# Optimization experiments

Hardware: AMD Instinct MI355X
Metric: run time of the kernel (lower is better)

Reference implementation:

```python
import jax, jax.numpy as jnp
import numpy as np

B, T, D, H = 2, 2048, 1024, 16
DH = D // H
THETA = 10000.0
MAX_SEQ_LEN = 2048


def setup_inputs() -> dict:
    key = jax.random.key(0)
    kx, kqkv, ko = jax.random.split(key, 3)
    # trunc_normal init matching the torch Linear (std=sqrt(2/(fan_in+fan_out)), clipped at 3 sigma)
    sigma_qkv = (2.0 / (D + 3 * D)) ** 0.5
    sigma_o = (2.0 / (D + D)) ** 0.5
    W_qkv = jax.random.truncated_normal(kqkv, -3.0, 3.0, (3 * D, D), jnp.float32) * sigma_qkv
    W_o = jax.random.truncated_normal(ko, -3.0, 3.0, (D, D), jnp.float32) * sigma_o
    # RoPE caches: angles[t, i] = t / theta^(2i/d_k)
    dims = jnp.arange(0, DH, 2, dtype=jnp.float32)
    inv_freq = 1.0 / (THETA ** (dims / DH))  # [DH/2]
    angles = jnp.arange(MAX_SEQ_LEN, dtype=jnp.float32)[:, None] * inv_freq[None, :]  # [T, DH/2]
    return {
        "x": jax.random.normal(kx, (B, T, D), jnp.float32),
        "token_positions": jnp.arange(T, dtype=jnp.int64 if jax.config.jax_enable_x64 else jnp.int32),
        "W_qkv": W_qkv,
        "W_o": W_o,
        "cos_cached": jnp.cos(angles),
        "sin_cached": jnp.sin(angles),
    }


def _apply_rope(x, cos, sin):
    # x: [b, h, t, dh]; cos/sin: [t, dh/2] broadcast over (b, h)
    x1 = x[..., 0::2]
    x2 = x[..., 1::2]
    r1 = x1 * cos - x2 * sin
    r2 = x1 * sin + x2 * cos
    # interleave back: (.., dh/2, 2) -> (.., dh)
    return jnp.stack([r1, r2], axis=-1).reshape(x.shape)


def reference(x, token_positions, W_qkv, W_o, cos_cached, sin_cached):
    b, t, d = x.shape
    qkv = jnp.einsum("btd,ed->bte", x, W_qkv)  # [b, t, 3d]
    q, k, v = jnp.split(qkv, 3, axis=-1)

    def to_heads(z):
        return z.reshape(b, t, H, DH).transpose(0, 2, 1, 3)  # [b, h, t, dh]

    q, k, v = to_heads(q), to_heads(k), to_heads(v)

    cos = cos_cached[token_positions]  # [t, dh/2]
    sin = sin_cached[token_positions]
    q = _apply_rope(q, cos, sin)
    k = _apply_rope(k, cos, sin)

    scale = 1.0 / jnp.sqrt(jnp.asarray(DH, x.dtype))
    scores = jnp.einsum("bhqd,bhkd->bhqk", q, k) * scale  # full TxT (naive, matches source)
    causal = jnp.tril(jnp.ones((t, t), dtype=bool))  # [t, t]
    scores = jnp.where(causal[None, None, :, :], scores, -jnp.inf)
    attn = jax.nn.softmax(scores, axis=-1)
    out = jnp.einsum("bhqk,bhkd->bhqd", attn, v)  # [b, h, t, dh]
    out = out.transpose(0, 2, 1, 3).reshape(b, t, d)
    return jnp.einsum("btd,ed->bte", out, W_o)
```

## Files before the change

kernel.cpp:

```cpp
#include <hip/hip_runtime.h>
#include <hip/hip_bf16.h>
#include <stdint.h>

#define Bn  2
#define Tn  2048
#define Dn  1024
#define Hn  16
#define DHn 64
#define QSCALE 0.1803368801111204f

typedef unsigned short u16;
typedef __attribute__((ext_vector_type(8))) short s16x8;
typedef __attribute__((ext_vector_type(8))) unsigned short u16x8;
typedef __attribute__((ext_vector_type(4))) unsigned short u16x4;
typedef __attribute__((ext_vector_type(4))) float f32x4;

#define MFMA(a, b, c) __builtin_amdgcn_mfma_f32_16x16x32_bf16((a), (b), (c), 0, 0, 0)

__device__ __forceinline__ u16 f2bf(float f) {
  union { __hip_bfloat16 b; u16 u; } c;
  c.b = __float2bfloat16(f);
  return c.u;
}
__device__ __forceinline__ float bf2f(u16 u) {
  union { u16 u; __hip_bfloat16 b; } c;
  c.u = u;
  return __bfloat162float(c.b);
}

__device__ __forceinline__ void lds16(void* lds, const void* g) {
  __builtin_amdgcn_global_load_lds((__attribute__((address_space(1))) void*)(g),
                                   (__attribute__((address_space(3))) void*)(lds), 16, 0, 0);
}

__global__ __launch_bounds__(256) void k_cvt2(const float* __restrict__ s0, int n0,
                                              const float* __restrict__ s1, int n1,
                                              u16* __restrict__ dst) {
  int i = blockIdx.x * blockDim.x + threadIdx.x;
  const int stride = gridDim.x * blockDim.x;
  const int nt = n0 + n1;
  for (; i < nt; i += stride) {
    float4 v = (i < n0) ? ((const float4*)s0)[i] : ((const float4*)s1)[i - n0];
    u16x4 o;
    o[0] = f2bf(v.x); o[1] = f2bf(v.y); o[2] = f2bf(v.z); o[3] = f2bf(v.w);
    ((u16x4*)dst)[i] = o;
  }
}

__global__ __launch_bounds__(256) void k_cvt(const float* __restrict__ src,
                                             u16* __restrict__ dst, int n4) {
  int i = blockIdx.x * blockDim.x + threadIdx.x;
  const int stride = gridDim.x * blockDim.x;
  for (; i < n4; i += stride) {
    float4 v = ((const float4*)src)[i];
    u16x4 o;
    o[0] = f2bf(v.x); o[1] = f2bf(v.y); o[2] = f2bf(v.z); o[3] = f2bf(v.w);
    ((u16x4*)dst)[i] = o;
  }
}

__global__ __launch_bounds__(256) void k_qkv(
    const u16* __restrict__ xb, const u16* __restrict__ wb,
    const int* __restrict__ tokpos,
    const float* __restrict__ cosc, const float* __restrict__ sinc,
    u16* __restrict__ qb, u16* __restrict__ kb, u16* __restrict__ vtb)
{
  __shared__ u16 smem[32768];
  const int tid  = threadIdx.x;
  const int bcol = blockIdx.x;
  const int brow = blockIdx.y;
  const int lane = tid & 63, w = tid >> 6;
  const int wr = w >> 1, wc = w & 1;
  const int l15 = lane & 15, l4 = lane >> 4;
  const int lrow = lane >> 3;
  const int gsw  = ((lane & 7) ^ (lane >> 3)) * 8;
  const int rsw  = l15 & 7;

  f32x4 acc[4][4] = {};

#pragma unroll
  for (int c = 0; c < 4; ++c) {
    const int r0 = w * 32 + c * 8;
    lds16(&smem[r0 * 64],         xb + (size_t)(brow * 128 + r0 + lrow) * 1024 + gsw);
    lds16(&smem[16384 + r0 * 64], wb + (size_t)(bcol * 128 + r0 + lrow) * 1024 + gsw);
  }

  for (int kt = 0; kt < 16; ++kt) {
    const int cur = kt & 1;
    const u16* Asb = smem + cur * 8192;
    const u16* Bsb = smem + 16384 + cur * 8192;
    if (kt < 15) {
      u16* Asn = smem + (cur ^ 1) * 8192;
      u16* Bsn = smem + 16384 + (cur ^ 1) * 8192;
      const int k1 = (kt + 1) * 64;
#pragma unroll
      for (int c = 0; c < 4; ++c) {
        const int r0 = w * 32 + c * 8;
        lds16(&Asn[r0 * 64], xb + (size_t)(brow * 128 + r0 + lrow) * 1024 + k1 + gsw);
        lds16(&Bsn[r0 * 64], wb + (size_t)(bcol * 128 + r0 + lrow) * 1024 + k1 + gsw);
      }
      asm volatile("s_waitcnt vmcnt(8)" ::: "memory");
    } else {
      asm volatile("s_waitcnt vmcnt(0)" ::: "memory");
    }
    __builtin_amdgcn_s_barrier();
    __builtin_amdgcn_sched_barrier(0);
    __builtin_amdgcn_s_setprio(1);
#pragma unroll
    for (int kk = 0; kk < 64; kk += 32) {
      const int gc = (kk >> 3) + l4;
      s16x8 af[4], bf[4];
#pragma unroll
      for (int m = 0; m < 4; ++m)
        af[m] = *(const s16x8*)&Asb[(wr * 64 + m * 16 + l15) * 64 + ((gc ^ rsw) * 8)];
#pragma unroll
      for (int n = 0; n < 4; ++n)
        bf[n] = *(const s16x8*)&Bsb[(wc * 64 + n * 16 + l15) * 64 + ((gc ^ rsw) * 8)];
#pragma unroll
      for (int m = 0; m < 4; ++m)
#pragma unroll
        for (int n = 0; n < 4; ++n)
          acc[m][n] = MFMA(af[m], bf[n], acc[m][n]);
    }
    __builtin_amdgcn_s_setprio(0);
    __builtin_amdgcn_sched_barrier(0);
    __builtin_amdgcn_s_barrier();
  }

#pragma unroll
  for (int m = 0; m < 4; ++m)
#pragma unroll
    for (int n = 0; n < 4; ++n)
#pragma unroll
      for (int r = 0; r < 4; ++r)
        smem[(wr * 64 + m * 16 + l4 * 4 + r) * 136 + wc * 64 + n * 16 + l15] =
            f2bf(acc[m][n][r]);
  __syncthreads();

  if (bcol < 16) {
    u16* dst; float sc;
    if (bcol < 8) { dst = qb; sc = QSCALE; } else { dst = kb; sc = 1.0f; }
#pragma unroll
    for (int ph = 0; ph < 8; ++ph) {
      const int task = ph * 256 + tid;
      const int lr   = task >> 4;
      const int cg   = task & 15;
      const int rowg = brow * 128 + lr;
      const int b = rowg >> 11, t = rowg & 2047;
      const int rem = (bcol * 128 + cg * 8) & 1023;
      const int h = rem >> 6, dh0 = rem & 63;
      u16x8 v = *(const u16x8*)&smem[lr * 136 + cg * 8];
      const int pos = tokpos[t];
      const float4 cv = *(const float4*)&cosc[pos * 32 + (dh0 >> 1)];
      const float4 sv = *(const float4*)&sinc[pos * 32 + (dh0 >> 1)];
      const float cc[4] = {cv.x, cv.y, cv.z, cv.w};
      const float ss[4] = {sv.x, sv.y, sv.z, sv.w};
      u16x8 o;
#pragma unroll
      for (int p = 0; p < 4; ++p) {
        const float x1 = bf2f(v[2 * p]), x2 = bf2f(v[2 * p + 1]);
        o[2 * p]     = f2bf((x1 * cc[p] - x2 * ss[p]) * sc);
        o[2 * p + 1] = f2bf((x1 * ss[p] + x2 * cc[p]) * sc);
      }
      *(u16x8*)(dst + ((size_t)(b * Hn + h) * Tn + t) * DHn + dh0) = o;
    }
  } else {
    const int b  = (brow * 128) >> 11;
    const int t0 = (brow * 128) & 2047;
#pragma unroll
    for (int ph = 0; ph < 8; ++ph) {
      const int task = ph * 256 + tid;
      const int col = task & 127;
      const int tg  = task >> 7;
      const int h  = 2 * (bcol - 16) + (col >> 6);
      const int dh = col & 63;
      u16x8 v;
#pragma unroll
      for (int j = 0; j < 8; ++j) v[j] = smem[(tg * 8 + j) * 136 + col];
      *(u16x8*)(vtb + ((size_t)(b * Hn + h) * DHn + dh) * Tn + t0 + tg * 8) = v;
    }
  }
}

__global__ __launch_bounds__(256) void k_attn(
    const u16* __restrict__ qbuf, const u16* __restrict__ kbuf,
    const u16* __restrict__ vtb, u16* __restrict__ ob)
{
  __shared__ u16 Ks[2][64][64];
  __shared__ u16 Vs[2][64][64];
  __shared__ u16 Ps[4][16][64];

  const int tid  = threadIdx.x;
  const int lane = tid & 63, w = tid >> 6;
  const int l15 = lane & 15, l4 = lane >> 4;
  const int lrow = lane >> 3;
  const int gsw  = ((lane & 7) ^ (lane >> 3)) * 8;
  const int rsw  = l15 & 7;

  const int lin  = blockIdx.x;
  const int bh   = lin & 31;
  const int qblk = 31 - (lin >> 5);
  const int b = bh >> 4, h = bh & 15;

  const u16* Qh = qbuf + (size_t)bh * Tn * DHn;
  const u16* Kh = kbuf + (size_t)bh * Tn * DHn;
  const u16* Vh = vtb  + (size_t)bh * DHn * Tn;

  const int q0 = qblk * 64 + w * 16;
  const int ntiles = qblk + 1;

  const s16x8 qf0 = *(const s16x8*)(Qh + (size_t)(q0 + l15) * 64 + l4 * 8);
  const s16x8 qf1 = *(const s16x8*)(Qh + (size_t)(q0 + l15) * 64 + 32 + l4 * 8);

  const s16x8 onesv = {(short)0x3F80, (short)0x3F80, (short)0x3F80, (short)0x3F80,
                       (short)0x3F80, (short)0x3F80, (short)0x3F80, (short)0x3F80};

  f32x4 o[4] = {};
  f32x4 o5 = {};
  float m = -3.0e38f;

  {
    const int r0 = w * 16;
    lds16(&Ks[0][r0][0],     Kh + (size_t)(r0 + lrow) * 64 + gsw);
    lds16(&Ks[0][r0 + 8][0], Kh + (size_t)(r0 + 8 + lrow) * 64 + gsw);
    lds16(&Vs[0][r0][0],     Vh + (size_t)(r0 + lrow) * Tn + gsw);
    lds16(&Vs[0][r0 + 8][0], Vh + (size_t)(r0 + 8 + lrow) * Tn + gsw);
  }

  for (int it = 0; it < ntiles; ++it) {
    const int buf = it & 1;
    if (it + 1 < ntiles) {
      const int nb = buf ^ 1;
      const int kv1 = (it + 1) * 64;
      const int r0 = w * 16;
      lds16(&Ks[nb][r0][0],     Kh + (size_t)(kv1 + r0 + lrow) * 64 + gsw);
      lds16(&Ks[nb][r0 + 8][0], Kh + (size_t)(kv1 + r0 + 8 + lrow) * 64 + gsw);
      lds16(&Vs[nb][r0][0],     Vh + (size_t)(r0 + lrow) * Tn + kv1 + gsw);
      lds16(&Vs[nb][r0 + 8][0], Vh + (size_t)(r0 + 8 + lrow) * Tn + kv1 + gsw);
      asm volatile("s_waitcnt vmcnt(4)" ::: "memory");
    } else {
      asm volatile("s_waitcnt vmcnt(0)" ::: "memory");
    }
    __builtin_amdgcn_s_barrier();
    __builtin_amdgcn_sched_barrier(0);

    f32x4 s[4] = {};
    __builtin_amdgcn_s_setprio(1);
#pragma unroll
    for (int ks = 0; ks < 2; ++ks) {
      const s16x8 qf = ks ? qf1 : qf0;
      const int gr = ((ks * 4 + l4) ^ rsw) * 8;
#pragma unroll
      for (int hh = 0; hh < 4; ++hh) {
        const s16x8 kf = *(const s16x8*)&Ks[buf][hh * 16 + l15][gr];
        s[hh] = MFMA(kf, qf, s[hh]);
      }
    }
    __builtin_amdgcn_s_setprio(0);

    if (it == ntiles - 1) {
      const int kvb = it * 64 + l4 * 4;
      const int qg  = q0 + l15;
#pragma unroll
      for (int hh = 0; hh < 4; ++hh)
#pragma unroll
        for (int rr = 0; rr < 4; ++rr)
          if (kvb + hh * 16 + rr > qg) s[hh][rr] = -3.0e38f;
    }

    const float a0 = fmaxf(fmaxf(s[0][0], s[0][1]), s[0][2]);
    const float a1 = fmaxf(fmaxf(s[0][3], s[1][0]), s[1][1]);
    const float a2 = fmaxf(fmaxf(s[1][2], s[1][3]), s[2][0]);
    const float a3 = fmaxf(fmaxf(s[2][1], s[2][2]), s[2][3]);
    const float a4 = fmaxf(fmaxf(s[3][0], s[3][1]), s[3][2]);
    float tmax = fmaxf(fmaxf(fmaxf(a0, a1), fmaxf(a2, a3)), fmaxf(a4, s[3][3]));
    tmax = fmaxf(tmax, __shfl_xor(tmax, 16));
    tmax = fmaxf(tmax, __shfl_xor(tmax, 32));

    if (__any(tmax > m + 8.0f)) {
      const float mn    = fmaxf(m, tmax);
      const float alpha = __builtin_amdgcn_exp2f(m - mn);
      m = mn;
#pragma unroll
      for (int n = 0; n < 4; ++n)
#pragma unroll
        for (int rr = 0; rr < 4; ++rr) o[n][rr] *= alpha;
#pragma unroll
      for (int rr = 0; rr < 4; ++rr) o5[rr] *= alpha;
    }

#pragma unroll
    for (int hh = 0; hh < 4; ++hh) {
      u16x4 pk;
#pragma unroll
      for (int rr = 0; rr < 4; ++rr)
        pk[rr] = f2bf(__builtin_amdgcn_exp2f(s[hh][rr] - m));
      const int pg = ((hh << 1) + (l4 >> 1)) ^ rsw;
      *(u16x4*)&Ps[w][l15][pg * 8 + (l4 & 1) * 4] = pk;
    }

    const s16x8 pf0 = *(const s16x8*)&Ps[w][l15][(l4 ^ rsw) * 8];
    const s16x8 pf1 = *(const s16x8*)&Ps[w][l15][((4 + l4) ^ rsw) * 8];

    __builtin_amdgcn_s_setprio(1);
#pragma unroll
    for (int n = 0; n < 4; ++n) {
      const int g0 = (l4 ^ rsw) * 8, g1 = ((4 + l4) ^ rsw) * 8;
      const s16x8 vf0 = *(const s16x8*)&Vs[buf][n * 16 + l15][g0];
      const s16x8 vf1 = *(const s16x8*)&Vs[buf][n * 16 + l15][g1];
      o[n] = MFMA(vf0, pf0, o[n]);
      o[n] = MFMA(vf1, pf1, o[n]);
    }
    o5 = MFMA(onesv, pf0, o5);
    o5 = MFMA(onesv, pf1, o5);
    __builtin_amdgcn_s_setprio(0);
    __builtin_amdgcn_sched_barrier(0);
    __builtin_amdgcn_s_barrier();
  }

  const float inv = 1.0f / o5[0];
  const int t = q0 + l15;
#pragma unroll
  for (int n = 0; n < 4; ++n) {
    u16x4 ov;
#pragma unroll
    for (int rr = 0; rr < 4; ++rr) ov[rr] = f2bf(o[n][rr] * inv);
    *(u16x4*)(ob + (size_t)(b * Tn + t) * Dn + h * 64 + n * 16 + l4 * 4) = ov;
  }
}

__global__ __launch_bounds__(256) void k_out(
    const u16* __restrict__ ob, const u16* __restrict__ wob,
    float* __restrict__ out)
{
  __shared__ u16 smem[24576];
  const int tid  = threadIdx.x;
  const int bcol = blockIdx.x;
  const int brow = blockIdx.y;
  const int lane = tid & 63, w = tid >> 6;
  const int wr = w >> 1, wc = w & 1;
  const int l15 = lane & 15, l4 = lane >> 4;
  const int lrow = lane >> 3;
  const int gsw  = ((lane & 7) ^ (lane >> 3)) * 8;
  const int rsw  = l15 & 7;

  f32x4 acc[4][2] = {};

#pragma unroll
  for (int c = 0; c < 4; ++c) {
    const int r0 = w * 32 + c * 8;
    lds16(&smem[r0 * 64], ob + (size_t)(brow * 128 + r0 + lrow) * 1024 + gsw);
  }
#pragma unroll
  for (int c = 0; c < 2; ++c) {
    const int r0 = w * 16 + c * 8;
    lds16(&smem[16384 + r0 * 64], wob + (size_t)(bcol * 64 + r0 + lrow) * 1024 + gsw);
  }

  for (int kt = 0; kt < 16; ++kt) {
    const int cur = kt & 1;
    const u16* Asb = smem + cur * 8192;
    const u16* Bsb = smem + 16384 + cur * 4096;
    if (kt < 15) {
      u16* Asn = smem + (cur ^ 1) * 8192;
      u16* Bsn = smem + 16384 + (cur ^ 1) * 4096;
      const int k1 = (kt + 1) * 64;
#pragma unroll
      for (int c = 0; c < 4; ++c) {
        const int r0 = w * 32 + c * 8;
        lds16(&Asn[r0 * 64], ob + (size_t)(brow * 128 + r0 + lrow) * 1024 + k1 + gsw);
      }
#pragma unroll
      for (int c = 0; c < 2; ++c) {
        const int r0 = w * 16 + c * 8;
        lds16(&Bsn[r0 * 64], wob + (size_t)(bcol * 64 + r0 + lrow) * 1024 + k1 + gsw);
      }
      asm volatile("s_waitcnt vmcnt(6)" ::: "memory");
    } else {
      asm volatile("s_waitcnt vmcnt(0)" ::: "memory");
    }
    __builtin_amdgcn_s_barrier();
    __builtin_amdgcn_sched_barrier(0);
    __builtin_amdgcn_s_setprio(1);
#pragma unroll
    for (int kk = 0; kk < 64; kk += 32) {
      const int gc = (kk >> 3) + l4;
      s16x8 af[4], bf[2];
#pragma unroll
      for (int m = 0; m < 4; ++m)
        af[m] = *(const s16x8*)&Asb[(wr * 64 + m * 16 + l15) * 64 + ((gc ^ rsw) * 8)];
#pragma unroll
      for (int n = 0; n < 2; ++n)
        bf[n] = *(const s16x8*)&Bsb[(wc * 32 + n * 16 + l15) * 64 + ((gc ^ rsw) * 8)];
#pragma unroll
      for (int m = 0; m < 4; ++m)
#pragma unroll
        for (int n = 0; n < 2; ++n)
          acc[m][n] = MFMA(af[m], bf[n], acc[m][n]);
    }
    __builtin_amdgcn_s_setprio(0);
    __builtin_amdgcn_sched_barrier(0);
    __builtin_amdgcn_s_barrier();
  }

#pragma unroll
  for (int m = 0; m < 4; ++m) {
    const int rowb = brow * 128 + wr * 64 + m * 16 + l4 * 4;
#pragma unroll
    for (int n = 0; n < 2; ++n) {
      const int colg = bcol * 64 + wc * 32 + n * 16 + l15;
#pragma unroll
      for (int r = 0; r < 4; ++r)
        out[(size_t)(rowb + r) * 1024 + colg] = acc[m][n][r];
    }
  }
}

extern "C" void kernel_launch(void* const* d_in, const int* in_sizes, int n_in,
                              void* d_out, int out_size, void* d_ws, size_t ws_size,
                              hipStream_t stream) {
  const float* x      = (const float*)d_in[0];
  const int*   tokpos = (const int*)d_in[1];
  const float* wqkv   = (const float*)d_in[2];
  const float* wo     = (const float*)d_in[3];
  const float* cosc   = (const float*)d_in[4];
  const float* sinc   = (const float*)d_in[5];
  float* out = (float*)d_out;

  u16* xb    = (u16*)d_ws;
  u16* wqkvb = xb + (size_t)Bn * Tn * Dn;
  u16* qb    = wqkvb + (size_t)3 * Dn * Dn;
  u16* kb    = qb + (size_t)Bn * Tn * Dn;
  u16* vtb   = kb + (size_t)Bn * Tn * Dn;
  u16* ob    = xb;
  u16* wob   = wqkvb;

  dim3 blk(256);
  k_cvt2<<<dim3(2048), blk, 0, stream>>>(x, (Bn * Tn * Dn) / 4,
                                         wqkv, (3 * Dn * Dn) / 4, xb);

  k_qkv<<<dim3(24, 32), blk, 0, stream>>>(xb, wqkvb, tokpos, cosc, sinc, qb, kb, vtb);

  k_cvt<<<dim3(1024), blk, 0, stream>>>(wo, wob, (Dn * Dn) / 4);

  k_attn<<<dim3(1024), blk, 0, stream>>>(qb, kb, vtb, ob);

  k_out<<<dim3(16, 32), blk, 0, stream>>>(ob, wob, out);
}
```

Measured before the change: 107.9 us.

## Halve QKV GEMM K-tile to shrink LDS and reorder attention block scheduling

The QKV projection GEMM now stages 32-wide K slices instead of 64-wide ones, with a matching 4-chunk XOR swizzle. This roughly halves the shared-memory footprint so more blocks can be resident per CU, at the cost of twice as many barrier-separated iterations. The attention kernel also replaces its longest-first query-block order with an interleaved ordering that mixes short and long causal rows across dispatch waves, aiming to balance load across CUs.

Measured after the change: 107.2 us. No clear change (-0.7%).

```diff
diff --git a/kernel.cpp b/kernel.cpp
--- a/kernel.cpp
+++ b/kernel.cpp
@@ -65,57 +65,59 @@
     const float* __restrict__ cosc, const float* __restrict__ sinc,
     u16* __restrict__ qb, u16* __restrict__ kb, u16* __restrict__ vtb)
 {
-  __shared__ u16 smem[32768];
+  __shared__ u16 smem[17408];
   const int tid  = threadIdx.x;
   const int bcol = blockIdx.x;
   const int brow = blockIdx.y;
   const int lane = tid & 63, w = tid >> 6;
   const int wr = w >> 1, wc = w & 1;
   const int l15 = lane & 15, l4 = lane >> 4;
-  const int lrow = lane >> 3;
-  const int gsw  = ((lane & 7) ^ (lane >> 3)) * 8;
-  const int rsw  = l15 & 7;
+  const int lrow = lane >> 2;
+  const int gsw  = (((lane & 3) ^ ((lrow >> 1) & 3)) * 8);
+  const int rsw  = (l15 >> 1) & 3;
+
+  const u16* xrow = xb + (size_t)(brow * 128) * 1024;
+  const u16* wrow = wb + (size_t)(bcol * 128) * 1024;
 
   f32x4 acc[4][4] = {};
 
-#pragma unroll
-  for (int c = 0; c < 4; ++c) {
-    const int r0 = w * 32 + c * 8;
-    lds16(&smem[r0 * 64],         xb + (size_t)(brow * 128 + r0 + lrow) * 1024 + gsw);
-    lds16(&smem[16384 + r0 * 64], wb + (size_t)(bcol * 128 + r0 + lrow) * 1024 + gsw);
-  }
-
-  for (int kt = 0; kt < 16; ++kt) {
+  {
+    const int r0 = w * 32;
+    lds16(&smem[r0 * 32],              xrow + (size_t)(r0 + lrow) * 1024 + gsw);
+    lds16(&smem[(r0 + 16) * 32],       xrow + (size_t)(r0 + 16 + lrow) * 1024 + gsw);
+    lds16(&smem[8192 + r0 * 32],       wrow + (size_t)(r0 + lrow) * 1024 + gsw);
+    lds16(&smem[8192 + (r0 + 16) * 32],wrow + (size_t)(r0 + 16 + lrow) * 1024 + gsw);
+  }
+
+  for (int kt = 0; kt < 32; ++kt) {
     const int cur = kt & 1;
-    const u16* Asb = smem + cur * 8192;
-    const u16* Bsb = smem + 16384 + cur * 8192;
-    if (kt < 15) {
-      u16* Asn = smem + (cur ^ 1) * 8192;
-      u16* Bsn = smem + 16384 + (cur ^ 1) * 8192;
-      const int k1 = (kt + 1) * 64;
-#pragma unroll
-      for (int c = 0; c < 4; ++c) {
-        const int r0 = w * 32 + c * 8;
-        lds16(&Asn[r0 * 64], xb + (size_t)(brow * 128 + r0 + lrow) * 1024 + k1 + gsw);
-        lds16(&Bsn[r0 * 64], wb + (size_t)(bcol * 128 + r0 + lrow) * 1024 + k1 + gsw);
-      }
-      asm volatile("s_waitcnt vmcnt(8)" ::: "memory");
+    const u16* Asb = smem + cur * 4096;
+    const u16* Bsb = smem + 8192 + cur * 4096;
+    if (kt < 31) {
+      u16* Asn = smem + (cur ^ 1) * 4096;
+      u16* Bsn = smem + 8192 + (cur ^ 1) * 4096;
+      const int k1 = (kt + 1) * 32;
+      const int r0 = w * 32;
+      lds16(&Asn[r0 * 32],        xrow + (size_t)(r0 + lrow) * 1024 + k1 + gsw);
+      lds16(&Asn[(r0 + 16) * 32], xrow + (size_t)(r0 + 16 + lrow) * 1024 + k1 + gsw);
+      lds16(&Bsn[r0 * 32],        wrow + (size_t)(r0 + lrow) * 1024 + k1 + gsw);
+      lds16(&Bsn[(r0 + 16) * 32], wrow + (size_t)(r0 + 16 + lrow) * 1024 + k1 + gsw);
+      asm volatile("s_waitcnt vmcnt(4)" ::: "memory");
     } else {
       asm volatile("s_waitcnt vmcnt(0)" ::: "memory");
     }
     __builtin_amdgcn_s_barrier();
     __builtin_amdgcn_sched_barrier(0);
     __builtin_amdgcn_s_setprio(1);
-#pragma unroll
-    for (int kk = 0; kk < 64; kk += 32) {
-      const int gc = (kk >> 3) + l4;
+    {
+      const int gr = (l4 ^ rsw) * 8;
       s16x8 af[4], bf[4];
 #pragma unroll
       for (int m = 0; m < 4; ++m)
-        af[m] = *(const s16x8*)&Asb[(wr * 64 + m * 16 + l15) * 64 + ((gc ^ rsw) * 8)];
+        af[m] = *(const s16x8*)&Asb[(wr * 64 + m * 16 + l15) * 32 + gr];
 #pragma unroll
       for (int n = 0; n < 4; ++n)
-        bf[n] = *(const s16x8*)&Bsb[(wc * 64 + n * 16 + l15) * 64 + ((gc ^ rsw) * 8)];
+        bf[n] = *(const s16x8*)&Bsb[(wc * 64 + n * 16 + l15) * 32 + gr];
 #pragma unroll
       for (int m = 0; m < 4; ++m)
 #pragma unroll
@@ -197,9 +199,10 @@
   const int gsw  = ((lane & 7) ^ (lane >> 3)) * 8;
   const int rsw  = l15 & 7;
 
-  const int lin  = blockIdx.x;
-  const int bh   = lin & 31;
-  const int qblk = 31 - (lin >> 5);
+  const int lin = blockIdx.x;
+  const int bh  = lin & 31;
+  const int a   = (lin >> 5) & 7, rb = lin >> 8;
+  const int qblk = (rb == 0) ? a : (rb == 1) ? (15 - a) : (rb == 2) ? (16 + a) : (31 - a);
   const int b = bh >> 4, h = bh & 15;
 
   const u16* Qh = qbuf + (size_t)bh * Tn * DHn;
```
